# Kernel optimization log

Measured on AMD Instinct MI355X. Metric: run time of the kernel, lower is better.

The kernel has to match this reference:

```python
import jax, jax.numpy as jnp
import numpy as np

B, T, H, Q = 64, 2048, 512, 512


def setup_inputs() -> dict:
    key = jax.random.key(0)
    k1, k2, k3, k4, k5 = jax.random.split(key, 5)
    query = jax.random.normal(k1, (B, Q), dtype=jnp.float32)
    encoder_outputs = jax.random.normal(k2, (B, T, H), dtype=jnp.float32)
    # nn.Linear(hidden_size, query_size): weight [Q, H], bias [Q]
    W = jax.random.normal(k3, (Q, H), dtype=jnp.float32) * (1.0 / np.sqrt(H))
    b = jax.random.normal(k4, (Q,), dtype=jnp.float32) * 0.01
    tgt_index = jax.random.randint(k5, (B,), 0, T, dtype=jnp.int64)
    return {"query": query, "encoder_outputs": encoder_outputs, "W": W, "b": b,
            "tgt_index": tgt_index}


def reference(query, encoder_outputs, W, b, tgt_index):
    # method == 'general': energy[b,i] = (W @ enc[b,i] + bias) . query[b]
    proj = jnp.einsum('bth,qh->btq', encoder_outputs, W) + b       # [B,T,Q]
    energies = jnp.einsum('btq,bq->bt', proj, query)               # [B,T]
    # ragged mask: position i valid iff i <= tgt_index[b] (this_len = tgt_index+1)
    mask = jnp.arange(T)[None, :] <= tgt_index[:, None]            # [B,T]
    logits = jnp.where(mask, energies, -jnp.inf)
    attn = jax.nn.softmax(logits, axis=-1)                         # [B,T]
    context = jnp.einsum('bt,bth->bh', attn, encoder_outputs)      # [B,H]
    return context
```

## Files before the change

### kernel.cpp

```cpp
#include <hip/hip_runtime.h>
#include <hip/hip_bf16.h>
#include <math.h>


#define B 64
#define T 2048
#define H 512
#define Q 512

__global__ void k_proj(const float* __restrict__ query,
                       const float* __restrict__ W,
                       const float* __restrict__ bias,
                       float* __restrict__ v,
                       float* __restrict__ c) {
    int b = blockIdx.x;
    int tid = threadIdx.x;
    __shared__ float sq[Q];
    sq[tid] = query[(size_t)b * Q + tid];
    __syncthreads();

    float acc = 0.0f;
#pragma unroll 8
    for (int q = 0; q < Q; ++q) {
        acc += sq[q] * W[(size_t)q * H + tid];
    }
    v[(size_t)b * H + tid] = acc;

    float pb = sq[tid] * bias[tid];
    for (int off = 32; off; off >>= 1) pb += __shfl_xor(pb, off, 64);
    __shared__ float sred[8];
    if ((tid & 63) == 0) sred[tid >> 6] = pb;
    __syncthreads();
    if (tid == 0) {
        float s = 0.0f;
        for (int i = 0; i < 8; ++i) s += sred[i];
        c[b] = s;
    }
}

#define TT 256
__global__ void k_energy(const float* __restrict__ enc,
                         const float* __restrict__ v,
                         const float* __restrict__ c,
                         const int* __restrict__ tgt,
                         float* __restrict__ e) {
    int b = blockIdx.y;
    int len = tgt[b] + 1;
    int t0 = blockIdx.x * TT;
    if (t0 >= len) return;

    __shared__ float sv[H];
    int tid = threadIdx.x;
    sv[tid]       = v[(size_t)b * H + tid];
    sv[tid + 256] = v[(size_t)b * H + 256 + tid];
    __syncthreads();

    int wave = tid >> 6;
    int lane = tid & 63;
    float cb = c[b];
    const float4* sv4 = (const float4*)sv;
    float4 w0 = sv4[lane];
    float4 w1 = sv4[lane + 64];

    int tend = min(t0 + TT, len);
    for (int t = t0 + wave; t < tend; t += 4) {
        const float4* row = (const float4*)(enc + ((size_t)b * T + t) * H);
        float4 a0 = row[lane];
        float4 a1 = row[lane + 64];
        float acc = a0.x * w0.x + a0.y * w0.y + a0.z * w0.z + a0.w * w0.w
                  + a1.x * w1.x + a1.y * w1.y + a1.z * w1.z + a1.w * w1.w;
        for (int off = 32; off; off >>= 1) acc += __shfl_xor(acc, off, 64);
        if (lane == 0) e[(size_t)b * T + t] = acc + cb;
    }
}

__global__ void k_softmax(const float* __restrict__ e,
                          const int* __restrict__ tgt,
                          float* __restrict__ p,
                          float* __restrict__ out) {
    int b = blockIdx.x;
    int len = tgt[b] + 1;
    int tid = threadIdx.x;

    out[(size_t)b * H + tid] = 0.0f;
    out[(size_t)b * H + 256 + tid] = 0.0f;

    __shared__ float red[256];

    float m = -INFINITY;
    for (int t = tid; t < len; t += 256) m = fmaxf(m, e[(size_t)b * T + t]);
    red[tid] = m;
    __syncthreads();
    for (int s = 128; s; s >>= 1) {
        if (tid < s) red[tid] = fmaxf(red[tid], red[tid + s]);
        __syncthreads();
    }
    m = red[0];
    __syncthreads();

    float s = 0.0f;
    for (int t = tid; t < len; t += 256) s += __expf(e[(size_t)b * T + t] - m);
    red[tid] = s;
    __syncthreads();
    for (int k = 128; k; k >>= 1) {
        if (tid < k) red[tid] += red[tid + k];
        __syncthreads();
    }
    float inv = 1.0f / red[0];

    for (int t = tid; t < len; t += 256)
        p[(size_t)b * T + t] = __expf(e[(size_t)b * T + t] - m) * inv;
}

__global__ void k_context(const float* __restrict__ enc,
                          const float* __restrict__ p,
                          const int* __restrict__ tgt,
                          float* __restrict__ out) {
    int b = blockIdx.y;
    int len = tgt[b] + 1;
    int t0 = blockIdx.x * TT;
    if (t0 >= len) return;
    int n = min(TT, len - t0);

    __shared__ float sp[TT];
    int tid = threadIdx.x;
    sp[tid] = (tid < n) ? p[(size_t)b * T + t0 + tid] : 0.0f;
    __syncthreads();

    float acc0 = 0.0f, acc1 = 0.0f;
    const float* base = enc + ((size_t)b * T + t0) * H;

    int i = 0;
    for (; i + 4 <= n; i += 4) {
        const float2* r0 = (const float2*)(base + (size_t)(i + 0) * H);
        const float2* r1 = (const float2*)(base + (size_t)(i + 1) * H);
        const float2* r2 = (const float2*)(base + (size_t)(i + 2) * H);
        const float2* r3 = (const float2*)(base + (size_t)(i + 3) * H);
        float2 x0 = r0[tid];
        float2 x1 = r1[tid];
        float2 x2 = r2[tid];
        float2 x3 = r3[tid];
        float w0 = sp[i], w1 = sp[i + 1], w2 = sp[i + 2], w3 = sp[i + 3];
        acc0 += w0 * x0.x + w1 * x1.x + w2 * x2.x + w3 * x3.x;
        acc1 += w0 * x0.y + w1 * x1.y + w2 * x2.y + w3 * x3.y;
    }
    for (; i < n; ++i) {
        const float2* r = (const float2*)(base + (size_t)i * H);
        float2 x = r[tid];
        float w = sp[i];
        acc0 += w * x.x;
        acc1 += w * x.y;
    }

    atomicAdd(&out[(size_t)b * H + 2 * tid], acc0);
    atomicAdd(&out[(size_t)b * H + 2 * tid + 1], acc1);
}

extern "C" void kernel_launch(void* const* d_in, const int* in_sizes, int n_in,
                              void* d_out, int out_size, void* d_ws, size_t ws_size,
                              hipStream_t stream) {
    const float* query = (const float*)d_in[0];
    const float* enc   = (const float*)d_in[1];
    const float* W     = (const float*)d_in[2];
    const float* bias  = (const float*)d_in[3];
    const int*   tgt   = (const int*)d_in[4];
    float* out = (float*)d_out;

    char* ws = (char*)d_ws;
    float* v = (float*)ws;                               ws += (size_t)B * H * sizeof(float);
    float* c = (float*)ws;                               ws += 256;
    float* e = (float*)ws;                               ws += (size_t)B * T * sizeof(float);
    float* p = (float*)ws;

    k_proj<<<dim3(B), dim3(512), 0, stream>>>(query, W, bias, v, c);
    k_energy<<<dim3(T / TT, B), dim3(256), 0, stream>>>(enc, v, c, tgt, e);
    k_softmax<<<dim3(B), dim3(256), 0, stream>>>(e, tgt, p, out);
    k_context<<<dim3(T / TT, B), dim3(256), 0, stream>>>(enc, p, tgt, out);
}
```

Measured before the change: 412.6 us.

## Fuse energy, softmax and context into single-pass online-softmax kernel

Replaces the separate energy, softmax and context kernels with one flash-style kernel. Each wavefront computes energies, keeps a running max and sum, and accumulates a weighted context over its rows, writing a per-wave partial. A small combine kernel then merges the partials, so the encoder tensor is read once instead of twice and the atomics on the output go away. The projection kernel is also split across more blocks for parallelism. In exchange it adds extra exp work per row and a partial-context buffer to write and re-read.

```diff
diff --git a/kernel.cpp b/kernel.cpp
--- a/kernel.cpp
+++ b/kernel.cpp
@@ -7,47 +7,51 @@
 #define T 2048
 #define H 512
 #define Q 512
+#define TT 128
+#define NCH (T / TT)
+#define NPW (NCH * 4)
 
 __global__ void k_proj(const float* __restrict__ query,
                        const float* __restrict__ W,
                        const float* __restrict__ bias,
                        float* __restrict__ v,
                        float* __restrict__ c) {
-    int b = blockIdx.x;
+    int b = blockIdx.y;
     int tid = threadIdx.x;
+    int h = blockIdx.x * 128 + tid;
+
     __shared__ float sq[Q];
-    sq[tid] = query[(size_t)b * Q + tid];
+    for (int i = tid; i < Q; i += 128) sq[i] = query[(size_t)b * Q + i];
     __syncthreads();
 
     float acc = 0.0f;
 #pragma unroll 8
-    for (int q = 0; q < Q; ++q) {
-        acc += sq[q] * W[(size_t)q * H + tid];
-    }
-    v[(size_t)b * H + tid] = acc;
+    for (int q = 0; q < Q; ++q) acc += sq[q] * W[(size_t)q * H + h];
+    v[(size_t)b * H + h] = acc;
 
-    float pb = sq[tid] * bias[tid];
-    for (int off = 32; off; off >>= 1) pb += __shfl_xor(pb, off, 64);
-    __shared__ float sred[8];
-    if ((tid & 63) == 0) sred[tid >> 6] = pb;
-    __syncthreads();
-    if (tid == 0) {
-        float s = 0.0f;
-        for (int i = 0; i < 8; ++i) s += sred[i];
-        c[b] = s;
+    if (blockIdx.x == 0) {
+        float pb = 0.0f;
+        for (int i = tid; i < Q; i += 128) pb += sq[i] * bias[i];
+        for (int off = 32; off; off >>= 1) pb += __shfl_xor(pb, off, 64);
+        __shared__ float sred[2];
+        if ((tid & 63) == 0) sred[tid >> 6] = pb;
+        __syncthreads();
+        if (tid == 0) c[b] = sred[0] + sred[1];
     }
 }
 
-#define TT 256
-__global__ void k_energy(const float* __restrict__ enc,
-                         const float* __restrict__ v,
-                         const float* __restrict__ c,
-                         const int* __restrict__ tgt,
-                         float* __restrict__ e) {
+__global__ __launch_bounds__(256) void k_attn(const float* __restrict__ enc,
+                                              const float* __restrict__ v,
+                                              const float* __restrict__ c,
+                                              const int* __restrict__ tgt,
+                                              float* __restrict__ pm,
+                                              float* __restrict__ pl,
+                                              float* __restrict__ pctx) {
     int b = blockIdx.y;
     int len = tgt[b] + 1;
     int t0 = blockIdx.x * TT;
     if (t0 >= len) return;
+    int n = min(TT, len - t0);
 
     __shared__ float sv[H];
     int tid = threadIdx.x;
@@ -57,103 +61,75 @@
 
     int wave = tid >> 6;
     int lane = tid & 63;
-    float cb = c[b];
     const float4* sv4 = (const float4*)sv;
     float4 w0 = sv4[lane];
     float4 w1 = sv4[lane + 64];
+    float cb = c[b];
 
-    int tend = min(t0 + TT, len);
-    for (int t = t0 + wave; t < tend; t += 4) {
-        const float4* row = (const float4*)(enc + ((size_t)b * T + t) * H);
-        float4 a0 = row[lane];
-        float4 a1 = row[lane + 64];
-        float acc = a0.x * w0.x + a0.y * w0.y + a0.z * w0.z + a0.w * w0.w
-                  + a1.x * w1.x + a1.y * w1.y + a1.z * w1.z + a1.w * w1.w;
-        for (int off = 32; off; off >>= 1) acc += __shfl_xor(acc, off, 64);
-        if (lane == 0) e[(size_t)b * T + t] = acc + cb;
+    float m = -INFINITY, l = 0.0f;
+    float4 a0 = {0.f, 0.f, 0.f, 0.f};
+    float4 a1 = {0.f, 0.f, 0.f, 0.f};
+
+    for (int t = wave; t < n; t += 4) {
+        const float4* row = (const float4*)(enc + ((size_t)b * T + t0 + t) * H);
+        float4 x0 = row[lane];
+        float4 x1 = row[lane + 64];
+        float e = x0.x * w0.x + x0.y * w0.y + x0.z * w0.z + x0.w * w0.w
+                + x1.x * w1.x + x1.y * w1.y + x1.z * w1.z + x1.w * w1.w;
+        for (int off = 32; off; off >>= 1) e += __shfl_xor(e, off, 64);
+        e += cb;
+
+        float mn = fmaxf(m, e);
+        float alpha = __expf(m - mn);
+        float p = __expf(e - mn);
+        l = l * alpha + p;
+        a0.x = a0.x * alpha + p * x0.x;
+        a0.y = a0.y * alpha + p * x0.y;
+        a0.z = a0.z * alpha + p * x0.z;
+        a0.w = a0.w * alpha + p * x0.w;
+        a1.x = a1.x * alpha + p * x1.x;
+        a1.y = a1.y * alpha + p * x1.y;
+        a1.z = a1.z * alpha + p * x1.z;
+        a1.w = a1.w * alpha + p * x1.w;
+        m = mn;
     }
+
+    int pidx = (b * NCH + blockIdx.x) * 4 + wave;
+    if (lane == 0) { pm[pidx] = m; pl[pidx] = l; }
+    float4* dst = (float4*)(pctx + (size_t)pidx * H);
+    dst[lane]      = a0;
+    dst[lane + 64] = a1;
 }
 
-__global__ void k_softmax(const float* __restrict__ e,
+__global__ void k_combine(const float* __restrict__ pm,
+                          const float* __restrict__ pl,
+                          const float* __restrict__ pctx,
                           const int* __restrict__ tgt,
-                          float* __restrict__ p,
                           float* __restrict__ out) {
     int b = blockIdx.x;
     int len = tgt[b] + 1;
+    int nch = (len + TT - 1) / TT;
+    int np = nch * 4;
+    int base = b * NPW;
     int tid = threadIdx.x;
 
-    out[(size_t)b * H + tid] = 0.0f;
-    out[(size_t)b * H + 256 + tid] = 0.0f;
-
-    __shared__ float red[256];
-
-    float m = -INFINITY;
-    for (int t = tid; t < len; t += 256) m = fmaxf(m, e[(size_t)b * T + t]);
-    red[tid] = m;
-    __syncthreads();
-    for (int s = 128; s; s >>= 1) {
-        if (tid < s) red[tid] = fmaxf(red[tid], red[tid + s]);
-        __syncthreads();
-    }
-    m = red[0];
-    __syncthreads();
-
-    float s = 0.0f;
-    for (int t = tid; t < len; t += 256) s += __expf(e[(size_t)b * T + t] - m);
-    red[tid] = s;
-    __syncthreads();
-    for (int k = 128; k; k >>= 1) {
-        if (tid < k) red[tid] += red[tid + k];
-        __syncthreads();
-    }
-    float inv = 1.0f / red[0];
-
-    for (int t = tid; t < len; t += 256)
-        p[(size_t)b * T + t] = __expf(e[(size_t)b * T + t] - m) * inv;
-}
-
-__global__ void k_context(const float* __restrict__ enc,
-                          const float* __restrict__ p,
-                          const int* __restrict__ tgt,
-                          float* __restrict__ out) {
-    int b = blockIdx.y;
-    int len = tgt[b] + 1;
-    int t0 = blockIdx.x * TT;
-    if (t0 >= len) return;
-    int n = min(TT, len - t0);
-
-    __shared__ float sp[TT];
-    int tid = threadIdx.x;
-    sp[tid] = (tid < n) ? p[(size_t)b * T + t0 + tid] : 0.0f;
-    __syncthreads();
+    float M = -INFINITY;
+    for (int j = 0; j < np; ++j) M = fmaxf(M, pm[base + j]);
+    float L = 0.0f;
+    for (int j = 0; j < np; ++j) L += pl[base + j] * __expf(pm[base + j] - M);
+    float invL = 1.0f / L;
 
     float acc0 = 0.0f, acc1 = 0.0f;
-    const float* base = enc + ((size_t)b * T + t0) * H;
-
-    int i = 0;
-    for (; i + 4 <= n; i += 4) {
-        const float2* r0 = (const float2*)(base + (size_t)(i + 0) * H);
-        const float2* r1 = (const float2*)(base + (size_t)(i + 1) * H);
-        const float2* r2 = (const float2*)(base + (size_t)(i + 2) * H);
-        const float2* r3 = (const float2*)(base + (size_t)(i + 3) * H);
-        float2 x0 = r0[tid];
-        float2 x1 = r1[tid];
-        float2 x2 = r2[tid];
-        float2 x3 = r3[tid];
-        float w0 = sp[i], w1 = sp[i + 1], w2 = sp[i + 2], w3 = sp[i + 3];
-        acc0 += w0 * x0.x + w1 * x1.x + w2 * x2.x + w3 * x3.x;
-        acc1 += w0 * x0.y + w1 * x1.y + w2 * x2.y + w3 * x3.y;
-    }
-    for (; i < n; ++i) {
-        const float2* r = (const float2*)(base + (size_t)i * H);
-        float2 x = r[tid];
-        float w = sp[i];
+    for (int j = 0; j < np; ++j) {
+        float mj = pm[base + j];
+        float w = (mj == -INFINITY) ? 0.0f : __expf(mj - M) * invL;
+        const float2* pc = (const float2*)(pctx + (size_t)(base + j) * H);
+        float2 x = pc[tid];
         acc0 += w * x.x;
         acc1 += w * x.y;
     }
-
-    atomicAdd(&out[(size_t)b * H + 2 * tid], acc0);
-    atomicAdd(&out[(size_t)b * H + 2 * tid + 1], acc1);
+    out[(size_t)b * H + 2 * tid]     = acc0;
+    out[(size_t)b * H + 2 * tid + 1] = acc1;
 }
 
 extern "C" void kernel_launch(void* const* d_in, const int* in_sizes, int n_in,
@@ -167,13 +143,13 @@
     float* out = (float*)d_out;
 
     char* ws = (char*)d_ws;
-    float* v = (float*)ws;                               ws += (size_t)B * H * sizeof(float);
-    float* c = (float*)ws;                               ws += 256;
-    float* e = (float*)ws;                               ws += (size_t)B * T * sizeof(float);
-    float* p = (float*)ws;
+    float* v    = (float*)ws;  ws += (size_t)B * H * sizeof(float);
+    float* c    = (float*)ws;  ws += 256;
+    float* pm   = (float*)ws;  ws += (size_t)B * NPW * sizeof(float);
+    float* pl   = (float*)ws;  ws += (size_t)B * NPW * sizeof(float);
+    float* pctx = (float*)ws;
 
-    k_proj<<<dim3(B), dim3(512), 0, stream>>>(query, W, bias, v, c);
-    k_energy<<<dim3(T / TT, B), dim3(256), 0, stream>>>(enc, v, c, tgt, e);
-    k_softmax<<<dim3(B), dim3(256), 0, stream>>>(e, tgt, p, out);
-    k_context<<<dim3(T / TT, B), dim3(256), 0, stream>>>(enc, p, tgt, out);
+    k_proj<<<dim3(H / 128, B), dim3(128), 0, stream>>>(query, W, bias, v, c);
+    k_attn<<<dim3(NCH, B), dim3(256), 0, stream>>>(enc, v, c, tgt, pm, pl, pctx);
+    k_combine<<<dim3(B), dim3(256), 0, stream>>>(pm, pl, pctx, tgt, out);
 }
```

After: 392.3 us. -4.9%, faster.
